# Kernel tuning notes

Measured on AMD Instinct MI355X. Metric: run time of the kernel, lower is better.

Reference implementation:

```python
import jax, jax.numpy as jnp
import numpy as np

D_MAX = 4                      # max_displacement
OUT_DIM = 2 * D_MAX + 1        # 9 -> 9**3 = 729 displacement offsets


def setup_inputs() -> dict:
    key = jax.random.key(0)
    k1, k2 = jax.random.split(key)
    shape = (1, 32, 48, 48, 48)  # (N, C, H, W, D)
    x1 = jax.random.normal(k1, shape, dtype=jnp.float32)
    x2 = jax.random.normal(k2, shape, dtype=jnp.float32)
    return {"x1": x1, "x2": x2}


def _correlation(x1, x2):
    N, C, H, W, D = x1.shape
    p = D_MAX
    # zero-pad x2 on all three spatial dims (matches F.pad([pad]*6))
    x2p = jnp.pad(x2, ((0, 0), (0, 0), (p, p), (p, p), (p, p)))
    # offsets in the same order as the torch triple loop: i (H) slowest, k (D) fastest
    r = jnp.arange(OUT_DIM)
    offs = jnp.stack(jnp.meshgrid(r, r, r, indexing="ij"), axis=-1).reshape(-1, 3)  # (729, 3)

    def corr_one(o):
        sl = jax.lax.dynamic_slice(x2p, (0, 0, o[0], o[1], o[2]), (N, C, H, W, D))
        return jnp.mean(x1 * sl, axis=1)  # (N, H, W, D) — mean over channels

    cv = jax.vmap(corr_one)(offs)          # (729, N, H, W, D)
    return jnp.transpose(cv, (1, 0, 2, 3, 4))  # (N, 729, H, W, D)


def reference(x1, x2):
    return _correlation(x1, x2)
```

## Files before the change

### kernel.cpp

```cpp
#include <hip/hip_runtime.h>
#include <stdint.h>


#define HH 48
#define WW 48
#define DD 48
#define PAD 4
#define OD 9
#define WT 4
#define PP 8
#define NDG 6
#define CCH 4
#define NCHUNK 8
#define X2POS 15
#define X2ROW 60
#define X2W 12
#define NACT 216
#define X2_FLOATS (CCH * X2W * X2ROW)
#define X1_FLOATS (CCH * WT * DD)
#define HWD (HH * WW * DD)
#define CHFLOATS (CCH * HWD)

#define GLOAD16(gp, lp)                                                  \
  __builtin_amdgcn_global_load_lds(                                      \
      (const __attribute__((address_space(1))) void*)(gp),               \
      (__attribute__((address_space(3))) void*)(lp), 16, 0, 0)

__global__ __launch_bounds__(256, 3) void corr_kernel(
    const float* __restrict__ x1,
    const float* __restrict__ x2,
    float* __restrict__ out) {

  __shared__ __attribute__((aligned(16))) float s_x2[2][X2_FLOATS];
  __shared__ __attribute__((aligned(16))) float s_x1[2][X1_FLOATS];

  const int wt = blockIdx.x;
  const int h  = blockIdx.y;
  const int i  = blockIdx.z;
  const int w0 = wt * WT;
  const int r  = h + i - PAD;
  const int t  = threadIdx.x;
  const int lane = t & 63;
  const int wv   = t >> 6;
  const bool row_ok = (r >= 0) & (r < HH);

  {
    const float4 z = make_float4(0.f, 0.f, 0.f, 0.f);
    float* p2 = &s_x2[0][0];
    for (int s = t; s < (2 * X2_FLOATS) / 4; s += 256)
      reinterpret_cast<float4*>(p2)[s] = z;
    float* p1 = &s_x1[0][0];
    for (int s = t; s < (2 * X1_FLOATS) / 4; s += 256)
      reinterpret_cast<float4*>(p1)[s] = z;
  }

  uint32_t o2[3];
  bool m2[3];
#pragma unroll
  for (int u = 0; u < 3; ++u) {
    const int m   = u * 64 + lane;
    const int w   = m / 15;
    const int pos = m - w * 15;
    const int wg  = w0 + w - PAD;
    m2[u] = (m < 180) & row_ok & ((unsigned)wg < (unsigned)WW) &
            ((unsigned)(pos - 1) < 12u);
    o2[u] = (uint32_t)(wv * HWD + r * (WW * DD) + wg * DD + (pos - 1) * 4);
  }
  const bool m1 = (lane < 48);
  const uint32_t o1 = (uint32_t)(wv * HWD + h * (WW * DD) + w0 * DD + lane * 4);

  int nvm = 1;
#pragma unroll
  for (int u = 0; u < 3; ++u) nvm += (__ballot(m2[u]) != 0ull) ? 1 : 0;

  const bool active = (t < NACT);
  int wl = 0, j = 0, dg = 0;
  if (active) {
    wl = t / (OD * NDG);
    int rem = t - wl * (OD * NDG);
    j = rem / NDG;
    dg = rem - j * NDG;
  }
  const int d0 = dg * PP;

  float acc[OD][PP];
#pragma unroll
  for (int k = 0; k < OD; ++k)
#pragma unroll
    for (int p = 0; p < PP; ++p) acc[k][p] = 0.0f;

  __syncthreads();

#pragma unroll
  for (int u = 0; u < 3; ++u)
    if (m2[u]) GLOAD16(x2 + o2[u], &s_x2[0][(wv * 180 + u * 64) * 4]);
  if (m1) GLOAD16(x1 + o1, &s_x1[0][(wv * 48) * 4]);

  for (int ch = 0; ch < NCHUNK; ++ch) {
    const int b = ch & 1;
    if (ch + 1 < NCHUNK) {
      const float* g2 = x2 + (size_t)(ch + 1) * CHFLOATS;
      const float* g1 = x1 + (size_t)(ch + 1) * CHFLOATS;
#pragma unroll
      for (int u = 0; u < 3; ++u)
        if (m2[u]) GLOAD16(g2 + o2[u], &s_x2[b ^ 1][(wv * 180 + u * 64) * 4]);
      if (m1) GLOAD16(g1 + o1, &s_x1[b ^ 1][(wv * 48) * 4]);
      switch (nvm) {
        case 4: asm volatile("s_waitcnt vmcnt(4)" ::: "memory"); break;
        case 3: asm volatile("s_waitcnt vmcnt(3)" ::: "memory"); break;
        case 2: asm volatile("s_waitcnt vmcnt(2)" ::: "memory"); break;
        default: asm volatile("s_waitcnt vmcnt(1)" ::: "memory"); break;
      }
    } else {
      asm volatile("s_waitcnt vmcnt(0)" ::: "memory");
    }
    __builtin_amdgcn_s_barrier();
    __builtin_amdgcn_sched_barrier(0);

    if (active) {
#pragma unroll
      for (int c = 0; c < CCH; ++c) {
        const float* px1 = &s_x1[b][c * (WT * DD) + wl * DD + d0];
        float xv[PP];
#pragma unroll
        for (int q = 0; q < 2; ++q) {
          const float4 v = *reinterpret_cast<const float4*>(px1 + q * 4);
          xv[q * 4 + 0] = v.x; xv[q * 4 + 1] = v.y;
          xv[q * 4 + 2] = v.z; xv[q * 4 + 3] = v.w;
        }
        const float* px2 = &s_x2[b][c * (X2W * X2ROW) + (wl + j) * X2ROW + d0];
        float win[PP + 8];
#pragma unroll
        for (int q = 0; q < 4; ++q) {
          const float4 v = *reinterpret_cast<const float4*>(px2 + q * 4);
          win[q * 4 + 0] = v.x; win[q * 4 + 1] = v.y;
          win[q * 4 + 2] = v.z; win[q * 4 + 3] = v.w;
        }
#pragma unroll
        for (int k = 0; k < OD; ++k)
#pragma unroll
          for (int p = 0; p < PP; ++p)
            acc[k][p] = fmaf(xv[p], win[p + k], acc[k][p]);
      }
    }
    __builtin_amdgcn_sched_barrier(0);
    __builtin_amdgcn_s_barrier();
    __builtin_amdgcn_sched_barrier(0);
  }

  if (active) {
    const float inv = 1.0f / 32.0f;
    const size_t spat = ((size_t)h * WW + (w0 + wl)) * DD + d0;
#pragma unroll
    for (int k = 0; k < OD; ++k) {
      const int o = (i * OD + j) * OD + k;
      float4 lo = make_float4(acc[k][0] * inv, acc[k][1] * inv,
                              acc[k][2] * inv, acc[k][3] * inv);
      float4 hi = make_float4(acc[k][4] * inv, acc[k][5] * inv,
                              acc[k][6] * inv, acc[k][7] * inv);
      float* dst = out + (size_t)o * (HH * WW * DD) + spat;
      *reinterpret_cast<float4*>(dst)     = lo;
      *reinterpret_cast<float4*>(dst + 4) = hi;
    }
  }
}

extern "C" void kernel_launch(void* const* d_in, const int* in_sizes, int n_in,
                              void* d_out, int out_size, void* d_ws, size_t ws_size,
                              hipStream_t stream) {
  const float* x1 = (const float*)d_in[0];
  const float* x2 = (const float*)d_in[1];
  float* out = (float*)d_out;
  dim3 grid(WW / WT, HH, OD);
  corr_kernel<<<grid, 256, 0, stream>>>(x1, x2, out);
}
```

Baseline: 400.1 us.

## Widen W tile to 8 and share x2 window across two output columns

Doubles the W tile per block to 8 columns and has each thread compute two adjacent output columns (w and w+1) that share the same x2 row window, using two accumulator sets. Each loaded x2 window feeds twice the FMAs, which cuts LDS reads per FMA, and each block loads a proportionally smaller halo. The cost is doubled accumulator registers (144 floats), lower occupancy (launch bounds 3->2), wasted edge work at jp=0/9, and a partially unrolled channel loop.

```diff
diff --git a/kernel.cpp b/kernel.cpp
--- a/kernel.cpp
+++ b/kernel.cpp
@@ -7,15 +7,16 @@
 #define DD 48
 #define PAD 4
 #define OD 9
-#define WT 4
+#define WT 8
 #define PP 8
-#define NDG 6
 #define CCH 4
 #define NCHUNK 8
 #define X2POS 15
 #define X2ROW 60
-#define X2W 12
-#define NACT 216
+#define X2W 16
+#define NACT 240
+#define X2UC 240
+#define X1UC 96
 #define X2_FLOATS (CCH * X2W * X2ROW)
 #define X1_FLOATS (CCH * WT * DD)
 #define HWD (HH * WW * DD)
@@ -26,7 +27,7 @@
       (const __attribute__((address_space(1))) void*)(gp),               \
       (__attribute__((address_space(3))) void*)(lp), 16, 0, 0)
 
-__global__ __launch_bounds__(256, 3) void corr_kernel(
+__global__ __launch_bounds__(256, 2) void corr_kernel(
     const float* __restrict__ x1,
     const float* __restrict__ x2,
     float* __restrict__ out) {
@@ -46,55 +47,66 @@
 
   {
     const float4 z = make_float4(0.f, 0.f, 0.f, 0.f);
-    float* p2 = &s_x2[0][0];
     for (int s = t; s < (2 * X2_FLOATS) / 4; s += 256)
-      reinterpret_cast<float4*>(p2)[s] = z;
-    float* p1 = &s_x1[0][0];
+      reinterpret_cast<float4*>(&s_x2[0][0])[s] = z;
     for (int s = t; s < (2 * X1_FLOATS) / 4; s += 256)
-      reinterpret_cast<float4*>(p1)[s] = z;
-  }
-
-  uint32_t o2[3];
-  bool m2[3];
-#pragma unroll
-  for (int u = 0; u < 3; ++u) {
+      reinterpret_cast<float4*>(&s_x1[0][0])[s] = z;
+  }
+
+  uint32_t o2[4];
+  bool m2[4];
+#pragma unroll
+  for (int u = 0; u < 4; ++u) {
     const int m   = u * 64 + lane;
-    const int w   = m / 15;
-    const int pos = m - w * 15;
+    const int w   = m / X2POS;
+    const int pos = m - w * X2POS;
     const int wg  = w0 + w - PAD;
-    m2[u] = (m < 180) & row_ok & ((unsigned)wg < (unsigned)WW) &
+    m2[u] = (m < X2UC) & row_ok & ((unsigned)wg < (unsigned)WW) &
             ((unsigned)(pos - 1) < 12u);
     o2[u] = (uint32_t)(wv * HWD + r * (WW * DD) + wg * DD + (pos - 1) * 4);
   }
-  const bool m1 = (lane < 48);
-  const uint32_t o1 = (uint32_t)(wv * HWD + h * (WW * DD) + w0 * DD + lane * 4);
-
-  int nvm = 1;
-#pragma unroll
-  for (int u = 0; u < 3; ++u) nvm += (__ballot(m2[u]) != 0ull) ? 1 : 0;
+  uint32_t o1[2];
+  bool m1[2];
+#pragma unroll
+  for (int u = 0; u < 2; ++u) {
+    const int m = u * 64 + lane;
+    m1[u] = (m < X1UC);
+    o1[u] = (uint32_t)(wv * HWD + h * (WW * DD) + w0 * DD + m * 4);
+  }
+
+  int nvm = 0;
+#pragma unroll
+  for (int u = 0; u < 4; ++u) nvm += (__ballot(m2[u]) != 0ull) ? 1 : 0;
+#pragma unroll
+  for (int u = 0; u < 2; ++u) nvm += (__ballot(m1[u]) != 0ull) ? 1 : 0;
 
   const bool active = (t < NACT);
-  int wl = 0, j = 0, dg = 0;
+  int q = 0, jp = 0, dg = 0;
   if (active) {
-    wl = t / (OD * NDG);
-    int rem = t - wl * (OD * NDG);
-    j = rem / NDG;
-    dg = rem - j * NDG;
+    q = t / 60;
+    int rem = t - q * 60;
+    jp = rem / 6;
+    dg = rem - jp * 6;
   }
   const int d0 = dg * PP;
-
-  float acc[OD][PP];
+  const int rr = 2 * q + jp;
+  const bool validA = active & (jp <= 8);
+  const bool validB = active & (jp >= 1);
+
+  float accA[OD][PP], accB[OD][PP];
 #pragma unroll
   for (int k = 0; k < OD; ++k)
 #pragma unroll
-    for (int p = 0; p < PP; ++p) acc[k][p] = 0.0f;
+    for (int p = 0; p < PP; ++p) { accA[k][p] = 0.0f; accB[k][p] = 0.0f; }
 
   __syncthreads();
 
 #pragma unroll
-  for (int u = 0; u < 3; ++u)
-    if (m2[u]) GLOAD16(x2 + o2[u], &s_x2[0][(wv * 180 + u * 64) * 4]);
-  if (m1) GLOAD16(x1 + o1, &s_x1[0][(wv * 48) * 4]);
+  for (int u = 0; u < 4; ++u)
+    if (m2[u]) GLOAD16(x2 + o2[u], &s_x2[0][(wv * X2UC + u * 64) * 4]);
+#pragma unroll
+  for (int u = 0; u < 2; ++u)
+    if (m1[u]) GLOAD16(x1 + o1[u], &s_x1[0][(wv * X1UC + u * 64) * 4]);
 
   for (int ch = 0; ch < NCHUNK; ++ch) {
     const int b = ch & 1;
@@ -102,10 +114,14 @@
       const float* g2 = x2 + (size_t)(ch + 1) * CHFLOATS;
       const float* g1 = x1 + (size_t)(ch + 1) * CHFLOATS;
 #pragma unroll
-      for (int u = 0; u < 3; ++u)
-        if (m2[u]) GLOAD16(g2 + o2[u], &s_x2[b ^ 1][(wv * 180 + u * 64) * 4]);
-      if (m1) GLOAD16(g1 + o1, &s_x1[b ^ 1][(wv * 48) * 4]);
+      for (int u = 0; u < 4; ++u)
+        if (m2[u]) GLOAD16(g2 + o2[u], &s_x2[b ^ 1][(wv * X2UC + u * 64) * 4]);
+#pragma unroll
+      for (int u = 0; u < 2; ++u)
+        if (m1[u]) GLOAD16(g1 + o1[u], &s_x1[b ^ 1][(wv * X1UC + u * 64) * 4]);
       switch (nvm) {
+        case 6: asm volatile("s_waitcnt vmcnt(6)" ::: "memory"); break;
+        case 5: asm volatile("s_waitcnt vmcnt(5)" ::: "memory"); break;
         case 4: asm volatile("s_waitcnt vmcnt(4)" ::: "memory"); break;
         case 3: asm volatile("s_waitcnt vmcnt(3)" ::: "memory"); break;
         case 2: asm volatile("s_waitcnt vmcnt(2)" ::: "memory"); break;
@@ -118,29 +134,34 @@
     __builtin_amdgcn_sched_barrier(0);
 
     if (active) {
-#pragma unroll
+#pragma unroll 2
       for (int c = 0; c < CCH; ++c) {
-        const float* px1 = &s_x1[b][c * (WT * DD) + wl * DD + d0];
-        float xv[PP];
-#pragma unroll
-        for (int q = 0; q < 2; ++q) {
-          const float4 v = *reinterpret_cast<const float4*>(px1 + q * 4);
-          xv[q * 4 + 0] = v.x; xv[q * 4 + 1] = v.y;
-          xv[q * 4 + 2] = v.z; xv[q * 4 + 3] = v.w;
+        const float* pw = &s_x2[b][c * (X2W * X2ROW) + rr * X2ROW + d0];
+        float win[PP + 8];
+#pragma unroll
+        for (int u = 0; u < 4; ++u) {
+          const float4 v = *reinterpret_cast<const float4*>(pw + u * 4);
+          win[u * 4 + 0] = v.x; win[u * 4 + 1] = v.y;
+          win[u * 4 + 2] = v.z; win[u * 4 + 3] = v.w;
         }
-        const float* px2 = &s_x2[b][c * (X2W * X2ROW) + (wl + j) * X2ROW + d0];
-        float win[PP + 8];
-#pragma unroll
-        for (int q = 0; q < 4; ++q) {
-          const float4 v = *reinterpret_cast<const float4*>(px2 + q * 4);
-          win[q * 4 + 0] = v.x; win[q * 4 + 1] = v.y;
-          win[q * 4 + 2] = v.z; win[q * 4 + 3] = v.w;
+        const float* pa = &s_x1[b][c * (WT * DD) + (2 * q) * DD + d0];
+        float xvA[PP], xvB[PP];
+#pragma unroll
+        for (int u = 0; u < 2; ++u) {
+          const float4 va = *reinterpret_cast<const float4*>(pa + u * 4);
+          xvA[u * 4 + 0] = va.x; xvA[u * 4 + 1] = va.y;
+          xvA[u * 4 + 2] = va.z; xvA[u * 4 + 3] = va.w;
+          const float4 vb = *reinterpret_cast<const float4*>(pa + DD + u * 4);
+          xvB[u * 4 + 0] = vb.x; xvB[u * 4 + 1] = vb.y;
+          xvB[u * 4 + 2] = vb.z; xvB[u * 4 + 3] = vb.w;
         }
 #pragma unroll
         for (int k = 0; k < OD; ++k)
 #pragma unroll
-          for (int p = 0; p < PP; ++p)
-            acc[k][p] = fmaf(xv[p], win[p + k], acc[k][p]);
+          for (int p = 0; p < PP; ++p) {
+            accA[k][p] = fmaf(xvA[p], win[p + k], accA[k][p]);
+            accB[k][p] = fmaf(xvB[p], win[p + k], accB[k][p]);
+          }
       }
     }
     __builtin_amdgcn_sched_barrier(0);
@@ -148,17 +169,31 @@
     __builtin_amdgcn_sched_barrier(0);
   }
 
-  if (active) {
-    const float inv = 1.0f / 32.0f;
-    const size_t spat = ((size_t)h * WW + (w0 + wl)) * DD + d0;
+  const float inv = 1.0f / 32.0f;
+  if (validA) {
+    const size_t spat = ((size_t)h * WW + (w0 + 2 * q)) * DD + d0;
 #pragma unroll
     for (int k = 0; k < OD; ++k) {
-      const int o = (i * OD + j) * OD + k;
-      float4 lo = make_float4(acc[k][0] * inv, acc[k][1] * inv,
-                              acc[k][2] * inv, acc[k][3] * inv);
-      float4 hi = make_float4(acc[k][4] * inv, acc[k][5] * inv,
-                              acc[k][6] * inv, acc[k][7] * inv);
-      float* dst = out + (size_t)o * (HH * WW * DD) + spat;
+      const int o = (i * OD + jp) * OD + k;
+      float4 lo = make_float4(accA[k][0] * inv, accA[k][1] * inv,
+                              accA[k][2] * inv, accA[k][3] * inv);
+      float4 hi = make_float4(accA[k][4] * inv, accA[k][5] * inv,
+                              accA[k][6] * inv, accA[k][7] * inv);
+      float* dst = out + (size_t)o * HWD + spat;
+      *reinterpret_cast<float4*>(dst)     = lo;
+      *reinterpret_cast<float4*>(dst + 4) = hi;
+    }
+  }
+  if (validB) {
+    const size_t spat = ((size_t)h * WW + (w0 + 2 * q + 1)) * DD + d0;
+#pragma unroll
+    for (int k = 0; k < OD; ++k) {
+      const int o = (i * OD + (jp - 1)) * OD + k;
+      float4 lo = make_float4(accB[k][0] * inv, accB[k][1] * inv,
+                              accB[k][2] * inv, accB[k][3] * inv);
+      float4 hi = make_float4(accB[k][4] * inv, accB[k][5] * inv,
+                              accB[k][6] * inv, accB[k][7] * inv);
+      float* dst = out + (size_t)o * HWD + spat;
       *reinterpret_cast<float4*>(dst)     = lo;
       *reinterpret_cast<float4*>(dst + 4) = hi;
     }
```

Result: no change. 407.4 us (+1.8%).
